# Kernel tuning notes

Hardware: AMD Instinct MI355X
Metric: run time of the kernel (lower is better)

## Reference

```python
import jax, jax.numpy as jnp
import numpy as np
import math

B, S, E, H = 2, 2048, 512, 8
D = E // H
EPS = 1e-6
MAXN = 1.0 - 1e-5  # stay strictly inside the Poincare ball


def _norm(x):
    return jnp.sqrt(jnp.clip(jnp.sum(x * x, axis=-1, keepdims=True), 1e-12))


def expmap0(u):
    n = _norm(u)
    return jnp.tanh(n) * u / n


def logmap0(x):
    n = _norm(x)
    return jnp.arctanh(jnp.clip(n, None, MAXN)) * x / n


def hlinear(x, W, b):
    # HLinear: Mobius matvec == expmap0(W @ logmap0(x)), tangent bias
    return expmap0(logmap0(x) @ W.T + b)


def _lbeta(a, b):
    return math.lgamma(a) + math.lgamma(b) - math.lgamma(a + b)


def setup_inputs() -> dict:
    key = jax.random.key(0)
    ks = jax.random.split(key, 6)

    def pt(k, shape):  # random points on the Poincare ball
        return expmap0(0.2 * jax.random.normal(k, shape, dtype=jnp.float32))

    return {
        "query": pt(ks[0], (B, S, E)),
        "key": pt(ks[1], (B, S, E)),
        "value": pt(ks[2], (B, S, E)),
        "Wq": jax.random.normal(ks[3], (E, E), jnp.float32) / math.sqrt(E),
        "Wk": jax.random.normal(ks[4], (E, E), jnp.float32) / math.sqrt(E),
        "Wv": jax.random.normal(ks[5], (E, E), jnp.float32) / math.sqrt(E),
        "bq": jnp.zeros((E,), jnp.float32),
        "bk": jnp.zeros((E,), jnp.float32),
        "bv": jnp.zeros((E,), jnp.float32),
        "scale_tau": jnp.zeros((1,), jnp.float32),
        "scale_gamma": jnp.zeros((1,), jnp.float32),
    }


def reference(query, key, value, Wq, Wk, Wv, bq, bk, bv, scale_tau, scale_gamma):
    # hyperbolic q/k/v projections, then split heads: [B,H,S,D]
    q = hlinear(query, Wq, bq).reshape(B, S, H, D).transpose(0, 2, 1, 3)
    k = hlinear(key, Wk, bk).reshape(B, S, H, D).transpose(0, 2, 1, 3)
    v = hlinear(value, Wv, bv).reshape(B, S, H, D).transpose(0, 2, 1, 3)

    # pairwise Poincare distance via norms + dot (no [S,S,D] intermediate)
    qn2 = jnp.sum(q * q, -1)                       # [B,H,S]
    kn2 = jnp.sum(k * k, -1)                       # [B,H,S]
    dot = jnp.einsum('bhid,bhjd->bhij', q, k)      # [B,H,S,S]
    sq = jnp.clip(qn2[..., :, None] + kn2[..., None, :] - 2.0 * dot, 0.0)
    denom = jnp.clip((1.0 - qn2)[..., :, None] * (1.0 - kn2)[..., None, :], EPS)
    dist = jnp.arccosh(jnp.clip(1.0 + 2.0 * sq / denom, 1.0 + 1e-7))

    # attention_similarity: -d / tau + gamma, tau = 1/exp(scale_tau)
    sim = -dist * jnp.exp(scale_tau[0]) + scale_gamma[0]

    # causal mask + 'exp' activation (masked_fill(-inf) then exp -> 0)
    mask = jnp.triu(jnp.ones((S, S), bool), 1)
    w = jnp.where(mask, 0.0, jnp.exp(sim))         # [B,H,S,S]

    # gyromidpoint: (1/2) (x) [sum_j w lam_j v_j / sum_j w (lam_j - 1)]
    vn2 = jnp.sum(v * v, -1)
    lam = 2.0 / jnp.clip(1.0 - vn2, EPS)           # [B,H,S]
    num = jnp.einsum('bhij,bhjd->bhid', w, v * lam[..., None])
    den = jnp.einsum('bhij,bhj->bhi', w, lam - 1.0)
    m = num / jnp.clip(den, EPS)[..., None]
    mn = _norm(m)
    mid = jnp.tanh(0.5 * jnp.arctanh(jnp.clip(mn, None, MAXN))) * m / mn

    # beta-concatenation of heads back to embed_dim
    beta_ratio = math.exp(_lbeta(E / 2.0, 0.5) - _lbeta(D / 2.0, 0.5))
    t = logmap0(mid) * beta_ratio                  # [B,H,S,D]
    t = t.transpose(0, 2, 1, 3).reshape(B, S, E)
    return expmap0(t)
```

## Files before the change

### kernel.cpp

```cpp
#include <hip/hip_runtime.h>
#include <cmath>

#define BB 2
#define SS 2048
#define EE 512
#define HH 8
#define DD 64

typedef unsigned short u16t;
typedef __bf16 bf16x8 __attribute__((ext_vector_type(8)));
typedef float f32x4 __attribute__((ext_vector_type(4)));

__device__ __forceinline__ float bf2f(u16t u){
    union{unsigned int i; float f;} c; c.i = ((unsigned int)u)<<16; return c.f;
}
__device__ __forceinline__ u16t f2bf(float x){
    union{float f; unsigned int i;} c; c.f = x;
    return (u16t)((c.i + 0x7fffu + ((c.i>>16)&1u))>>16);
}
__device__ __forceinline__ float fast_tanh(float x){
    float e = __expf(2.f*x); return 1.f - 2.f/(e+1.f);
}
__device__ __forceinline__ float fast_atanh(float x){
    return 0.5f*__logf((1.f+x)/(1.f-x));
}
__device__ __forceinline__ f32x4 mfma16(bf16x8 a, bf16x8 b, f32x4 c){
    return __builtin_amdgcn_mfma_f32_16x16x32_bf16(a,b,c,0,0,0);
}
__device__ __forceinline__ int chunk_off(int qi){
    int g = qi >> 3;
    return (g==1) ? 2*(qi-8) : ((g==2) ? 16 + 3*(qi-16) : 40 + 4*(qi-24));
}

__global__ __launch_bounds__(256) void k_pre(const float* __restrict__ qp,
                                             const float* __restrict__ kp,
                                             const float* __restrict__ vp,
                                             u16t* __restrict__ Tlog,
                                             const float* __restrict__ Wq,
                                             const float* __restrict__ Wk,
                                             const float* __restrict__ Wv,
                                             u16t* __restrict__ Wb){
    int bx = blockIdx.x;
    if (bx < 3072){
        int gr = bx*4 + (threadIdx.x>>6);
        int t = gr >> 12;
        int row = gr & 4095;
        int lane = threadIdx.x & 63;
        const float* src = (t==0 ? qp : (t==1 ? kp : vp)) + (size_t)row*EE;
        const float4* s4 = (const float4*)(src + lane*8);
        float4 a = s4[0], b = s4[1];
        float x[8] = {a.x,a.y,a.z,a.w,b.x,b.y,b.z,b.w};
        float p = 0.f;
        #pragma unroll
        for (int i=0;i<8;++i) p += x[i]*x[i];
        #pragma unroll
        for (int off=32; off>=1; off>>=1) p += __shfl_xor(p, off, 64);
        float n = sqrtf(fmaxf(p, 1e-12f));
        float f = fast_atanh(fminf(n, 1.0f-1e-5f)) / n;
        u16t yb[8];
        #pragma unroll
        for (int i=0;i<8;++i) yb[i] = f2bf(f*x[i]);
        uint4 o;
        o.x = (unsigned)yb[0] | ((unsigned)yb[1]<<16);
        o.y = (unsigned)yb[2] | ((unsigned)yb[3]<<16);
        o.z = (unsigned)yb[4] | ((unsigned)yb[5]<<16);
        o.w = (unsigned)yb[6] | ((unsigned)yb[7]<<16);
        *(uint4*)(Tlog + ((size_t)(t*4096+row)*EE + lane*8)) = o;
    } else {
        int idx = ((bx-3072)*256 + threadIdx.x)*4;
        int t = idx >> 18;
        int off = idx & 262143;
        const float* W = (t==0 ? Wq : (t==1 ? Wk : Wv));
        float4 a = *(const float4*)(W + off);
        uint2 o;
        o.x = (unsigned)f2bf(a.x) | ((unsigned)f2bf(a.y)<<16);
        o.y = (unsigned)f2bf(a.z) | ((unsigned)f2bf(a.w)<<16);
        *(uint2*)(Wb + idx) = o;
    }
}

__global__ __launch_bounds__(256) void k_proj(const u16t* __restrict__ Tlog,
                                              const u16t* __restrict__ Wb,
                                              const float* __restrict__ bq,
                                              const float* __restrict__ bk,
                                              const float* __restrict__ bv,
                                              u16t* __restrict__ U){
    __shared__ __align__(16) u16t Wl[64][72];
    int bx = blockIdx.x;
    int t = bx >> 9; int rem = bx & 511;
    int m0 = (rem >> 3) << 6; int n0 = (rem & 7) << 6;
    int tid = threadIdx.x; int wv = tid>>6; int lane = tid&63;
    int l15 = lane & 15; int l4 = lane >> 4;
    const u16t* Tt = Tlog + (size_t)t*4096*EE;
    const u16t* Wt = Wb + (size_t)t*EE*EE;
    const float* bias = (t==0 ? bq : (t==1 ? bk : bv));
    f32x4 z = {0.f,0.f,0.f,0.f};
    f32x4 acc[4] = {z,z,z,z};
    int arow = m0 + 16*wv + l15;
    for (int ks=0; ks<8; ++ks){
        int k0 = ks*64;
        __syncthreads();
        {
            int rr = tid >> 2; int cc = (tid & 3) * 16;
            const uint4* g = (const uint4*)(Wt + (size_t)(n0+rr)*EE + k0 + cc);
            uint4 w0 = g[0], w1 = g[1];
            *(uint4*)&Wl[rr][cc]   = w0;
            *(uint4*)&Wl[rr][cc+8] = w1;
        }
        __syncthreads();
        bf16x8 a0 = *(const bf16x8*)(Tt + (size_t)arow*EE + k0 + l4*8);
        bf16x8 a1 = *(const bf16x8*)(Tt + (size_t)arow*EE + k0 + 32 + l4*8);
        #pragma unroll
        for (int f=0; f<4; ++f){
            bf16x8 b0 = *(const bf16x8*)&Wl[f*16+l15][l4*8];
            bf16x8 b1 = *(const bf16x8*)&Wl[f*16+l15][32+l4*8];
            acc[f] = mfma16(a0, b0, acc[f]);
            acc[f] = mfma16(a1, b1, acc[f]);
        }
    }
    u16t* Ut = U + (size_t)t*4096*EE;
    #pragma unroll
    for (int f=0; f<4; ++f){
        int col = n0 + f*16 + l15;
        float bs = bias[col];
        #pragma unroll
        for (int r=0; r<4; ++r){
            int row = m0 + 16*wv + l4*4 + r;
            Ut[(size_t)row*EE + col] = f2bf(acc[f][r] + bs);
        }
    }
}

__global__ __launch_bounds__(256) void k_expmap_split(const u16t* __restrict__ U,
        u16t* __restrict__ Q, u16t* __restrict__ K, u16t* __restrict__ VT,
        float* __restrict__ qn2, float* __restrict__ kn2, float* __restrict__ lam1){
    int gr = blockIdx.x*4 + (threadIdx.x>>6);
    int t = gr >> 12;
    int row = gr & 4095;
    int b = row >> 11; int s = row & 2047;
    int lane = threadIdx.x & 63;
    const u16t* u = U + ((size_t)t*4096 + row)*EE;
    uint4 raw = *(const uint4*)(u + lane*8);
    const u16t* rs = (const u16t*)&raw;
    float x[8];
    #pragma unroll
    for (int i=0;i<8;++i) x[i] = bf2f(rs[i]);
    float p = 0.f;
    #pragma unroll
    for (int i=0;i<8;++i) p += x[i]*x[i];
    #pragma unroll
    for (int off=32; off>=1; off>>=1) p += __shfl_xor(p, off, 64);
    float n = sqrtf(fmaxf(p, 1e-12f));
    float f = fast_tanh(n)/n;
    float y[8]; u16t yb[8];
    float hp = 0.f;
    #pragma unroll
    for (int i=0;i<8;++i){
        yb[i] = f2bf(f*x[i]);
        y[i]  = bf2f(yb[i]);
        hp += y[i]*y[i];
    }
    #pragma unroll
    for (int off=1; off<8; off<<=1) hp += __shfl_xor(hp, off, 64);
    hp = fminf(hp, 0.99999988f);
    int h = lane >> 3;
    size_t ih = (size_t)(b*HH + h)*SS + s;
    if (t == 0){
        uint4 o;
        o.x=(unsigned)yb[0]|((unsigned)yb[1]<<16); o.y=(unsigned)yb[2]|((unsigned)yb[3]<<16);
        o.z=(unsigned)yb[4]|((unsigned)yb[5]<<16); o.w=(unsigned)yb[6]|((unsigned)yb[7]<<16);
        *(uint4*)(Q + ih*DD + (lane&7)*8) = o;
        if ((lane&7)==0) qn2[ih] = hp;
    } else if (t == 1){
        uint4 o;
        o.x=(unsigned)yb[0]|((unsigned)yb[1]<<16); o.y=(unsigned)yb[2]|((unsigned)yb[3]<<16);
        o.z=(unsigned)yb[4]|((unsigned)yb[5]<<16); o.w=(unsigned)yb[6]|((unsigned)yb[7]<<16);
        *(uint4*)(K + ih*DD + (lane&7)*8) = o;
        if ((lane&7)==0) kn2[ih] = hp;
    } else {
        float lam = 2.f / fmaxf(1.f - hp, 1e-6f);
        size_t bh = (size_t)(b*HH + h);
        int d0 = (lane&7)*8;
        #pragma unroll
        for (int i=0;i<8;++i)
            VT[(bh*DD + d0 + i)*SS + s] = f2bf(y[i]*lam);
        if ((lane&7)==0) lam1[ih] = lam - 1.f;
    }
}

__global__ __launch_bounds__(256,5) void k_attn(const u16t* __restrict__ Q,
        const u16t* __restrict__ K, const u16t* __restrict__ VT,
        const float* __restrict__ qn2, const float* __restrict__ kn2,
        const float* __restrict__ lam1, const float* __restrict__ taup,
        const float* __restrict__ gammap,
        float* __restrict__ pnum, float* __restrict__ pden,
        float* __restrict__ T2, float beta){
    __shared__ __align__(16) u16t Kt[64][72];
    __shared__ __align__(16) u16t Vt[64][72];
    __shared__ __align__(16) u16t Wt[64][72];
    __shared__ float kn2s[64], lam1s[64], qn2s[64];
    int bx = blockIdx.x;
    int bh = bx & 15;
    int u = bx >> 4;
    int qi, c0;
    if (u < 48){
        int g = u >> 3, r = u & 7;
        int qb = (g==0) ? 8 : ((g<3) ? 16 : 24);
        int cb = (g==0) ? 0 : ((g<3) ? (g-1) : (g-3));
        qi = qb + r; c0 = cb;
    } else {
        int p = u - 48;
        qi = (7 - (p>>2)) + ((p&3)<<3);
        c0 = qi >> 3;
    }
    int jt0 = c0 << 3;
    int jt1 = (u < 48) ? (jt0 + 8) : (qi + 1);
    int s0 = qi << 6;
    int tid = threadIdx.x; int wv = tid>>6; int lane = tid&63;
    int l15 = lane & 15; int l4 = lane >> 4;
    float tauexp = __expf(taup[0]);
    float gm2 = gammap[0] * 1.44269504088896340736f;
    size_t base = (size_t)bh * SS;
    int qrow = s0 + 16*wv + l15;
    bf16x8 aQ0 = *(const bf16x8*)(Q + (base + qrow)*DD + l4*8);
    bf16x8 aQ1 = *(const bf16x8*)(Q + (base + qrow)*DD + 32 + l4*8);
    if (tid < 64) qn2s[tid] = qn2[base + s0 + tid];
    __syncthreads();
    int mloc0 = 16*wv + l4*4;
    float qv_[4], aq2_[4];
    #pragma unroll
    for (int r=0;r<4;++r){
        qv_[r]  = qn2s[mloc0+r];
        aq2_[r] = 2.f * __builtin_amdgcn_rcpf(fmaxf(1.f - qv_[r], 1e-6f));
    }
    f32x4 z4 = {0.f,0.f,0.f,0.f};
    f32x4 num[4] = {z4,z4,z4,z4};
    float den[4] = {0.f,0.f,0.f,0.f};
    int rr = tid >> 2; int cc = (tid & 3) << 4;
    uint4 pka0, pka1, pva0, pva1; float pkn = 0.f, pl1 = 0.f;
    {
        int kv0 = jt0 << 6;
        const uint4* gk = (const uint4*)(K + (base + kv0 + rr)*DD + cc);
        pka0 = gk[0]; pka1 = gk[1];
        const uint4* gv = (const uint4*)(VT + ((size_t)bh*DD + rr)*SS + kv0 + cc);
        pva0 = gv[0]; pva1 = gv[1];
        if (tid < 64){ pkn = kn2[base+kv0+tid]; pl1 = lam1[base+kv0+tid]; }
    }
    for (int jt=jt0; jt<jt1; ++jt){
        *(uint4*)&Kt[rr][cc]   = pka0;
        *(uint4*)&Kt[rr][cc+8] = pka1;
        *(uint4*)&Vt[rr][cc]   = pva0;
        *(uint4*)&Vt[rr][cc+8] = pva1;
        if (tid < 64){ kn2s[tid] = pkn; lam1s[tid] = pl1; }
        __syncthreads();
        if (jt+1 < jt1){
            int kv0n = (jt+1) << 6;
            const uint4* gk = (const uint4*)(K + (base + kv0n + rr)*DD + cc);
            pka0 = gk[0]; pka1 = gk[1];
            const uint4* gv = (const uint4*)(VT + ((size_t)bh*DD + rr)*SS + kv0n + cc);
            pva0 = gv[0]; pva1 = gv[1];
            if (tid < 64){ pkn = kn2[base+kv0n+tid]; pl1 = lam1[base+kv0n+tid]; }
        }
        int kv0 = jt << 6;
        f32x4 c[4] = {z4,z4,z4,z4};
        #pragma unroll
        for (int f=0; f<4; ++f){
            bf16x8 b0 = *(const bf16x8*)&Kt[f*16+l15][l4*8];
            bf16x8 b1 = *(const bf16x8*)&Kt[f*16+l15][32+l4*8];
            c[f] = mfma16(aQ0, b0, c[f]);
            c[f] = mfma16(aQ1, b1, c[f]);
        }
        bool diag = (jt == qi);
        #pragma unroll
        for (int f=0; f<4; ++f){
            int nl = f*16 + l15;
            float kv2 = kn2s[nl];
            float l1  = lam1s[nl];
            float akf = __builtin_amdgcn_rcpf(fmaxf(1.f - kv2, 1e-6f));
            #pragma unroll
            for (int r=0; r<4; ++r){
                int ml = mloc0 + r;
                float sq  = fmaxf(fmaf(-2.f, c[f][r], qv_[r] + kv2), 0.f);
                float co  = fminf(aq2_[r]*akf, 2e6f);
                float rho = fmaxf(sq*co, 1e-7f);
                float tt  = fmaf(rho, rho, rho+rho);
                float zz  = 1.f + rho + __builtin_amdgcn_sqrtf(tt);
                float L   = __builtin_amdgcn_logf(zz);
                float wval= __builtin_amdgcn_exp2f(fmaf(-tauexp, L, gm2));
                if (diag && (kv0+nl) > (s0+ml)) wval = 0.f;
                den[r] = fmaf(wval, l1, den[r]);
                Wt[ml][nl] = f2bf(wval);
            }
        }
        bf16x8 aW0 = *(const bf16x8*)&Wt[16*wv + l15][l4*8];
        bf16x8 aW1 = *(const bf16x8*)&Wt[16*wv + l15][32 + l4*8];
        #pragma unroll
        for (int f=0; f<4; ++f){
            bf16x8 b0 = *(const bf16x8*)&Vt[f*16+l15][l4*8];
            bf16x8 b1 = *(const bf16x8*)&Vt[f*16+l15][32+l4*8];
            num[f] = mfma16(aW0, b0, num[f]);
            num[f] = mfma16(aW1, b1, num[f]);
        }
        __syncthreads();
    }
    #pragma unroll
    for (int r=0; r<4; ++r){
        #pragma unroll
        for (int off=1; off<16; off<<=1) den[r] += __shfl_xor(den[r], off, 64);
    }
    if (qi >= 8){
        size_t pidx = (size_t)bh*72 + chunk_off(qi) + c0;
        float* pn = pnum + pidx*4096;
        #pragma unroll
        for (int f=0; f<4; ++f){
            int nl = f*16 + l15;
            #pragma unroll
            for (int r=0; r<4; ++r)
                pn[(mloc0+r)*64 + nl] = num[f][r];
        }
        if (l15 == 0){
            #pragma unroll
            for (int r=0; r<4; ++r) pden[pidx*64 + mloc0 + r] = den[r];
        }
    } else {
        float mv[4][4]; float mn2[4] = {0.f,0.f,0.f,0.f};
        #pragma unroll
        for (int f=0; f<4; ++f)
            #pragma unroll
            for (int r=0; r<4; ++r){
                mv[f][r] = num[f][r] / fmaxf(den[r], 1e-6f);
                mn2[r] += mv[f][r]*mv[f][r];
            }
        #pragma unroll
        for (int r=0; r<4; ++r){
            #pragma unroll
            for (int off=1; off<16; off<<=1) mn2[r] += __shfl_xor(mn2[r], off, 64);
        }
        int b = bh >> 3; int h = bh & 7;
        #pragma unroll
        for (int r=0; r<4; ++r){
            float mn = sqrtf(fmaxf(mn2[r], 1e-12f));
            float g = beta * 0.5f * fast_atanh(fminf(mn, 1.0f-1e-5f)) / mn;
            int ml = mloc0 + r;
            #pragma unroll
            for (int f=0; f<4; ++f){
                int nl = f*16 + l15;
                T2[((size_t)b*SS + s0 + ml)*EE + h*DD + nl] = g * mv[f][r];
            }
        }
    }
}

__global__ __launch_bounds__(256) void k_combine(const float* __restrict__ pnum,
        const float* __restrict__ pden, float* __restrict__ T2, float beta){
    int bx = blockIdx.x;
    int bh = bx & 15; int qi = 8 + (bx >> 4);
    int nch = (qi >> 3) + 1;
    int t = threadIdx.x; int row = t >> 2; int qd = t & 3;
    size_t pb = (size_t)bh*72 + chunk_off(qi);
    float mv[16];
    #pragma unroll
    for (int i=0;i<16;++i) mv[i] = 0.f;
    float den = 0.f;
    for (int cc=0; cc<nch; ++cc){
        const float* pn = pnum + (pb+cc)*4096 + row*64 + qd*16;
        #pragma unroll
        for (int i=0;i<4;++i){
            float4 v = *(const float4*)(pn + i*4);
            mv[i*4+0]+=v.x; mv[i*4+1]+=v.y; mv[i*4+2]+=v.z; mv[i*4+3]+=v.w;
        }
        den += pden[(pb+cc)*64 + row];
    }
    float invd = 1.f / fmaxf(den, 1e-6f);
    float mn2 = 0.f;
    #pragma unroll
    for (int i=0;i<16;++i){ mv[i] *= invd; mn2 += mv[i]*mv[i]; }
    mn2 += __shfl_xor(mn2, 1, 64);
    mn2 += __shfl_xor(mn2, 2, 64);
    float mn = sqrtf(fmaxf(mn2, 1e-12f));
    float g = beta * 0.5f * fast_atanh(fminf(mn, 1.0f-1e-5f)) / mn;
    int b = bh >> 3, h = bh & 7;
    float* dst = T2 + ((size_t)b*SS + (qi<<6) + row)*EE + h*DD + qd*16;
    #pragma unroll
    for (int i=0;i<4;++i){
        float4 v = {g*mv[i*4+0], g*mv[i*4+1], g*mv[i*4+2], g*mv[i*4+3]};
        *(float4*)(dst + i*4) = v;
    }
}

__global__ __launch_bounds__(256) void k_final(const float* __restrict__ T2,
                                               float* __restrict__ out){
    int row = blockIdx.x*4 + (threadIdx.x>>6);
    int lane = threadIdx.x & 63;
    const float* src = T2 + (size_t)row*EE;
    const float4* s4 = (const float4*)(src + lane*8);
    float4 a = s4[0], b = s4[1];
    float x[8] = {a.x,a.y,a.z,a.w,b.x,b.y,b.z,b.w};
    float p = 0.f;
    #pragma unroll
    for (int i=0;i<8;++i) p += x[i]*x[i];
    #pragma unroll
    for (int off=32; off>=1; off>>=1) p += __shfl_xor(p, off, 64);
    float n = sqrtf(fmaxf(p, 1e-12f));
    float f = fast_tanh(n)/n;
    float4 o0 = {f*x[0], f*x[1], f*x[2], f*x[3]};
    float4 o1 = {f*x[4], f*x[5], f*x[6], f*x[7]};
    float4* d4 = (float4*)(out + (size_t)row*EE + lane*8);
    d4[0] = o0; d4[1] = o1;
}

extern "C" void kernel_launch(void* const* d_in, const int* in_sizes, int n_in,
                              void* d_out, int out_size, void* d_ws, size_t ws_size,
                              hipStream_t stream) {
    const float* q_in  = (const float*)d_in[0];
    const float* k_in  = (const float*)d_in[1];
    const float* v_in  = (const float*)d_in[2];
    const float* Wq    = (const float*)d_in[3];
    const float* Wk    = (const float*)d_in[4];
    const float* Wv    = (const float*)d_in[5];
    const float* bq    = (const float*)d_in[6];
    const float* bk    = (const float*)d_in[7];
    const float* bv    = (const float*)d_in[8];
    const float* tau   = (const float*)d_in[9];
    const float* gamma = (const float*)d_in[10];
    float* out = (float*)d_out;

    char* ws = (char*)d_ws;
    u16t*  Tlog = (u16t*)(ws + 0);
    u16t*  Wb   = (u16t*)(ws + 12582912);
    u16t*  Ub   = (u16t*)(ws + 14155776);
    u16t*  Qb   = (u16t*)(ws + 26738688);
    u16t*  Kb   = (u16t*)(ws + 30932992);
    u16t*  VTb  = (u16t*)(ws + 35127296);
    float* qn2  = (float*)(ws + 39321600);
    float* kn2  = (float*)(ws + 39452672);
    float* lam1 = (float*)(ws + 39583744);
    float* pnum = (float*)(ws + 0);
    float* pden = (float*)(ws + 18874368);
    float* T2   = (float*)(ws + 39714816);

    double lb1 = std::lgamma(256.0) + std::lgamma(0.5) - std::lgamma(256.5);
    double lb2 = std::lgamma(32.0)  + std::lgamma(0.5) - std::lgamma(32.5);
    float beta = (float)std::exp(lb1 - lb2);

    k_pre<<<3840, 256, 0, stream>>>(q_in, k_in, v_in, Tlog, Wq, Wk, Wv, Wb);
    k_proj<<<1536, 256, 0, stream>>>(Tlog, Wb, bq, bk, bv, Ub);
    k_expmap_split<<<3072, 256, 0, stream>>>(Ub, Qb, Kb, VTb, qn2, kn2, lam1);
    k_attn<<<1280, 256, 0, stream>>>(Qb, Kb, VTb, qn2, kn2, lam1, tau, gamma,
                                     pnum, pden, T2, beta);
    k_combine<<<384, 256, 0, stream>>>(pnum, pden, T2, beta);
    k_final<<<1024, 256, 0, stream>>>(T2, out);
}
```

Measured before the change: 97.49 us.

## Split attention into 4-tile KV chunks, read K/V directly, prefetch W in projection

```diff
diff --git a/kernel.cpp b/kernel.cpp
--- a/kernel.cpp
+++ b/kernel.cpp
@@ -27,9 +27,9 @@
 __device__ __forceinline__ f32x4 mfma16(bf16x8 a, bf16x8 b, f32x4 c){
     return __builtin_amdgcn_mfma_f32_16x16x32_bf16(a,b,c,0,0,0);
 }
-__device__ __forceinline__ int chunk_off(int qi){
-    int g = qi >> 3;
-    return (g==1) ? 2*(qi-8) : ((g==2) ? 16 + 3*(qi-16) : 40 + 4*(qi-24));
+__device__ __forceinline__ int coff4(int qi){
+    int a = qi >> 2, b = qi & 3;
+    return 2*a*(a+1) - 4 + b*(a+1);
 }
 
 __global__ __launch_bounds__(256) void k_pre(const float* __restrict__ qp,
@@ -97,17 +97,21 @@
     f32x4 z = {0.f,0.f,0.f,0.f};
     f32x4 acc[4] = {z,z,z,z};
     int arow = m0 + 16*wv + l15;
+    int rr = tid >> 2; int cc = (tid & 3) * 16;
+    uint4 w0, w1;
+    {
+        const uint4* g = (const uint4*)(Wt + (size_t)(n0+rr)*EE + cc);
+        w0 = g[0]; w1 = g[1];
+    }
     for (int ks=0; ks<8; ++ks){
         int k0 = ks*64;
+        *(uint4*)&Wl[rr][cc]   = w0;
+        *(uint4*)&Wl[rr][cc+8] = w1;
         __syncthreads();
-        {
-            int rr = tid >> 2; int cc = (tid & 3) * 16;
-            const uint4* g = (const uint4*)(Wt + (size_t)(n0+rr)*EE + k0 + cc);
-            uint4 w0 = g[0], w1 = g[1];
-            *(uint4*)&Wl[rr][cc]   = w0;
-            *(uint4*)&Wl[rr][cc+8] = w1;
-        }
-        __syncthreads();
+        if (ks < 7){
+            const uint4* g = (const uint4*)(Wt + (size_t)(n0+rr)*EE + k0 + 64 + cc);
+            w0 = g[0]; w1 = g[1];
+        }
         bf16x8 a0 = *(const bf16x8*)(Tt + (size_t)arow*EE + k0 + l4*8);
         bf16x8 a1 = *(const bf16x8*)(Tt + (size_t)arow*EE + k0 + 32 + l4*8);
         #pragma unroll
@@ -117,6 +121,7 @@
             acc[f] = mfma16(a0, b0, acc[f]);
             acc[f] = mfma16(a1, b1, acc[f]);
         }
+        __syncthreads();
     }
     u16t* Ut = U + (size_t)t*4096*EE;
     #pragma unroll
@@ -188,33 +193,31 @@
     }
 }
 
-__global__ __launch_bounds__(256,5) void k_attn(const u16t* __restrict__ Q,
+__global__ __launch_bounds__(256,6) void k_attn(const u16t* __restrict__ Q,
         const u16t* __restrict__ K, const u16t* __restrict__ VT,
         const float* __restrict__ qn2, const float* __restrict__ kn2,
         const float* __restrict__ lam1, const float* __restrict__ taup,
         const float* __restrict__ gammap,
         float* __restrict__ pnum, float* __restrict__ pden,
         float* __restrict__ T2, float beta){
-    __shared__ __align__(16) u16t Kt[64][72];
-    __shared__ __align__(16) u16t Vt[64][72];
     __shared__ __align__(16) u16t Wt[64][72];
-    __shared__ float kn2s[64], lam1s[64], qn2s[64];
     int bx = blockIdx.x;
     int bh = bx & 15;
     int u = bx >> 4;
     int qi, c0;
-    if (u < 48){
-        int g = u >> 3, r = u & 7;
-        int qb = (g==0) ? 8 : ((g<3) ? 16 : 24);
-        int cb = (g==0) ? 0 : ((g<3) ? (g-1) : (g-3));
-        qi = qb + r; c0 = cb;
+    if (u < 140){
+        int v = 139 - u;
+        int a = 1;
+        while (2*(a+1)*(a+2)-4 <= v) ++a;
+        int rem = v - (2*a*(a+1)-4);
+        int b_ = rem / (a+1);
+        c0 = rem - b_*(a+1);
+        qi = 4*a + b_;
     } else {
-        int p = u - 48;
-        qi = (7 - (p>>2)) + ((p&3)<<3);
-        c0 = qi >> 3;
-    }
-    int jt0 = c0 << 3;
-    int jt1 = (u < 48) ? (jt0 + 8) : (qi + 1);
+        qi = u - 140; c0 = 0;
+    }
+    int jt0 = c0 << 2;
+    int jt1 = min(jt0 + 4, qi + 1);
     int s0 = qi << 6;
     int tid = threadIdx.x; int wv = tid>>6; int lane = tid&63;
     int l15 = lane & 15; int l4 = lane >> 4;
@@ -224,58 +227,43 @@
     int qrow = s0 + 16*wv + l15;
     bf16x8 aQ0 = *(const bf16x8*)(Q + (base + qrow)*DD + l4*8);
     bf16x8 aQ1 = *(const bf16x8*)(Q + (base + qrow)*DD + 32 + l4*8);
-    if (tid < 64) qn2s[tid] = qn2[base + s0 + tid];
-    __syncthreads();
     int mloc0 = 16*wv + l4*4;
     float qv_[4], aq2_[4];
     #pragma unroll
     for (int r=0;r<4;++r){
-        qv_[r]  = qn2s[mloc0+r];
+        qv_[r]  = qn2[base + s0 + mloc0 + r];
         aq2_[r] = 2.f * __builtin_amdgcn_rcpf(fmaxf(1.f - qv_[r], 1e-6f));
     }
     f32x4 z4 = {0.f,0.f,0.f,0.f};
     f32x4 num[4] = {z4,z4,z4,z4};
     float den[4] = {0.f,0.f,0.f,0.f};
-    int rr = tid >> 2; int cc = (tid & 3) << 4;
-    uint4 pka0, pka1, pva0, pva1; float pkn = 0.f, pl1 = 0.f;
-    {
-        int kv0 = jt0 << 6;
-        const uint4* gk = (const uint4*)(K + (base + kv0 + rr)*DD + cc);
-        pka0 = gk[0]; pka1 = gk[1];
-        const uint4* gv = (const uint4*)(VT + ((size_t)bh*DD + rr)*SS + kv0 + cc);
-        pva0 = gv[0]; pva1 = gv[1];
-        if (tid < 64){ pkn = kn2[base+kv0+tid]; pl1 = lam1[base+kv0+tid]; }
-    }
     for (int jt=jt0; jt<jt1; ++jt){
-        *(uint4*)&Kt[rr][cc]   = pka0;
-        *(uint4*)&Kt[rr][cc+8] = pka1;
-        *(uint4*)&Vt[rr][cc]   = pva0;
-        *(uint4*)&Vt[rr][cc+8] = pva1;
-        if (tid < 64){ kn2s[tid] = pkn; lam1s[tid] = pl1; }
-        __syncthreads();
-        if (jt+1 < jt1){
-            int kv0n = (jt+1) << 6;
-            const uint4* gk = (const uint4*)(K + (base + kv0n + rr)*DD + cc);
-            pka0 = gk[0]; pka1 = gk[1];
-            const uint4* gv = (const uint4*)(VT + ((size_t)bh*DD + rr)*SS + kv0n + cc);
-            pva0 = gv[0]; pva1 = gv[1];
-            if (tid < 64){ pkn = kn2[base+kv0n+tid]; pl1 = lam1[base+kv0n+tid]; }
-        }
         int kv0 = jt << 6;
+        const u16t* Kp = K + (base + kv0)*DD;
+        const u16t* Vp = VT + ((size_t)bh*DD)*SS + kv0;
+        float kn2v[4], l1v[4];
         f32x4 c[4] = {z4,z4,z4,z4};
         #pragma unroll
         for (int f=0; f<4; ++f){
-            bf16x8 b0 = *(const bf16x8*)&Kt[f*16+l15][l4*8];
-            bf16x8 b1 = *(const bf16x8*)&Kt[f*16+l15][32+l4*8];
-            c[f] = mfma16(aQ0, b0, c[f]);
-            c[f] = mfma16(aQ1, b1, c[f]);
+            kn2v[f] = kn2[base + kv0 + f*16 + l15];
+            l1v[f]  = lam1[base + kv0 + f*16 + l15];
+            bf16x8 kb0 = *(const bf16x8*)(Kp + (f*16+l15)*DD + l4*8);
+            bf16x8 kb1 = *(const bf16x8*)(Kp + (f*16+l15)*DD + 32 + l4*8);
+            c[f] = mfma16(aQ0, kb0, c[f]);
+            c[f] = mfma16(aQ1, kb1, c[f]);
+        }
+        bf16x8 vb0[4], vb1[4];
+        #pragma unroll
+        for (int f=0; f<4; ++f){
+            vb0[f] = *(const bf16x8*)(Vp + (size_t)(f*16+l15)*SS + l4*8);
+            vb1[f] = *(const bf16x8*)(Vp + (size_t)(f*16+l15)*SS + 32 + l4*8);
         }
         bool diag = (jt == qi);
         #pragma unroll
         for (int f=0; f<4; ++f){
             int nl = f*16 + l15;
-            float kv2 = kn2s[nl];
-            float l1  = lam1s[nl];
+            float kv2 = kn2v[f];
+            float l1  = l1v[f];
             float akf = __builtin_amdgcn_rcpf(fmaxf(1.f - kv2, 1e-6f));
             #pragma unroll
             for (int r=0; r<4; ++r){
@@ -296,20 +284,17 @@
         bf16x8 aW1 = *(const bf16x8*)&Wt[16*wv + l15][32 + l4*8];
         #pragma unroll
         for (int f=0; f<4; ++f){
-            bf16x8 b0 = *(const bf16x8*)&Vt[f*16+l15][l4*8];
-            bf16x8 b1 = *(const bf16x8*)&Vt[f*16+l15][32+l4*8];
-            num[f] = mfma16(aW0, b0, num[f]);
-            num[f] = mfma16(aW1, b1, num[f]);
-        }
-        __syncthreads();
+            num[f] = mfma16(aW0, vb0[f], num[f]);
+            num[f] = mfma16(aW1, vb1[f], num[f]);
+        }
     }
     #pragma unroll
     for (int r=0; r<4; ++r){
         #pragma unroll
         for (int off=1; off<16; off<<=1) den[r] += __shfl_xor(den[r], off, 64);
     }
-    if (qi >= 8){
-        size_t pidx = (size_t)bh*72 + chunk_off(qi) + c0;
+    if (qi >= 4){
+        size_t pidx = (size_t)bh*140 + coff4(qi) + c0;
         float* pn = pnum + pidx*4096;
         #pragma unroll
         for (int f=0; f<4; ++f){
@@ -354,10 +339,10 @@
 __global__ __launch_bounds__(256) void k_combine(const float* __restrict__ pnum,
         const float* __restrict__ pden, float* __restrict__ T2, float beta){
     int bx = blockIdx.x;
-    int bh = bx & 15; int qi = 8 + (bx >> 4);
-    int nch = (qi >> 3) + 1;
+    int bh = bx & 15; int qi = 4 + (bx >> 4);
+    int nch = (qi >> 2) + 1;
     int t = threadIdx.x; int row = t >> 2; int qd = t & 3;
-    size_t pb = (size_t)bh*72 + chunk_off(qi);
+    size_t pb = (size_t)bh*140 + coff4(qi);
     float mv[16];
     #pragma unroll
     for (int i=0;i<16;++i) mv[i] = 0.f;
@@ -435,9 +420,9 @@
     float* qn2  = (float*)(ws + 39321600);
     float* kn2  = (float*)(ws + 39452672);
     float* lam1 = (float*)(ws + 39583744);
-    float* pnum = (float*)(ws + 0);
-    float* pden = (float*)(ws + 18874368);
-    float* T2   = (float*)(ws + 39714816);
+    float* pnum = (float*)(ws + 39714816);
+    float* pden = (float*)(ws + 76414976);
+    float* T2   = (float*)(ws + 76988416);
 
     double lb1 = std::lgamma(256.0) + std::lgamma(0.5) - std::lgamma(256.5);
     double lb2 = std::lgamma(32.0)  + std::lgamma(0.5) - std::lgamma(32.5);
@@ -446,8 +431,8 @@
     k_pre<<<3840, 256, 0, stream>>>(q_in, k_in, v_in, Tlog, Wq, Wk, Wv, Wb);
     k_proj<<<1536, 256, 0, stream>>>(Tlog, Wb, bq, bk, bv, Ub);
     k_expmap_split<<<3072, 256, 0, stream>>>(Ub, Qb, Kb, VTb, qn2, kn2, lam1);
-    k_attn<<<1280, 256, 0, stream>>>(Qb, Kb, VTb, qn2, kn2, lam1, tau, gamma,
+    k_attn<<<2304, 256, 0, stream>>>(Qb, Kb, VTb, qn2, kn2, lam1, tau, gamma,
                                      pnum, pden, T2, beta);
-    k_combine<<<384, 256, 0, stream>>>(pnum, pden, T2, beta);
+    k_combine<<<448, 256, 0, stream>>>(pnum, pden, T2, beta);
     k_final<<<1024, 256, 0, stream>>>(T2, out);
 }
```

New measurement: 156.6 us. 1.61x slower.

## Use 128-row query tiles in attention and fuse combine with final expmap

Applied to the files above, without the earlier changes.

```diff
diff --git a/kernel.cpp b/kernel.cpp
--- a/kernel.cpp
+++ b/kernel.cpp
@@ -27,9 +27,10 @@
 __device__ __forceinline__ f32x4 mfma16(bf16x8 a, bf16x8 b, f32x4 c){
     return __builtin_amdgcn_mfma_f32_16x16x32_bf16(a,b,c,0,0,0);
 }
-__device__ __forceinline__ int chunk_off(int qi){
-    int g = qi >> 3;
-    return (g==1) ? 2*(qi-8) : ((g==2) ? 16 + 3*(qi-16) : 40 + 4*(qi-24));
+__device__ __forceinline__ int nch128(int qb){ return (qb+2)>>1; }
+__device__ __forceinline__ int off128(int qb){
+    int m = qb>>1;
+    return (qb & 1) ? (m+1)*(m+1) : m*(m+1);
 }
 
 __global__ __launch_bounds__(256) void k_pre(const float* __restrict__ qp,
@@ -97,17 +98,21 @@
     f32x4 z = {0.f,0.f,0.f,0.f};
     f32x4 acc[4] = {z,z,z,z};
     int arow = m0 + 16*wv + l15;
+    int rr = tid >> 2; int cc = (tid & 3) * 16;
+    uint4 w0, w1;
+    {
+        const uint4* g = (const uint4*)(Wt + (size_t)(n0+rr)*EE + cc);
+        w0 = g[0]; w1 = g[1];
+    }
     for (int ks=0; ks<8; ++ks){
         int k0 = ks*64;
+        *(uint4*)&Wl[rr][cc]   = w0;
+        *(uint4*)&Wl[rr][cc+8] = w1;
         __syncthreads();
-        {
-            int rr = tid >> 2; int cc = (tid & 3) * 16;
-            const uint4* g = (const uint4*)(Wt + (size_t)(n0+rr)*EE + k0 + cc);
-            uint4 w0 = g[0], w1 = g[1];
-            *(uint4*)&Wl[rr][cc]   = w0;
-            *(uint4*)&Wl[rr][cc+8] = w1;
-        }
-        __syncthreads();
+        if (ks < 7){
+            const uint4* g = (const uint4*)(Wt + (size_t)(n0+rr)*EE + k0 + 64 + cc);
+            w0 = g[0]; w1 = g[1];
+        }
         bf16x8 a0 = *(const bf16x8*)(Tt + (size_t)arow*EE + k0 + l4*8);
         bf16x8 a1 = *(const bf16x8*)(Tt + (size_t)arow*EE + k0 + 32 + l4*8);
         #pragma unroll
@@ -117,6 +122,7 @@
             acc[f] = mfma16(a0, b0, acc[f]);
             acc[f] = mfma16(a1, b1, acc[f]);
         }
+        __syncthreads();
     }
     u16t* Ut = U + (size_t)t*4096*EE;
     #pragma unroll
@@ -188,54 +194,48 @@
     }
 }
 
-__global__ __launch_bounds__(256,5) void k_attn(const u16t* __restrict__ Q,
+__global__ __launch_bounds__(256,3) void k_attn(const u16t* __restrict__ Q,
         const u16t* __restrict__ K, const u16t* __restrict__ VT,
         const float* __restrict__ qn2, const float* __restrict__ kn2,
         const float* __restrict__ lam1, const float* __restrict__ taup,
         const float* __restrict__ gammap,
-        float* __restrict__ pnum, float* __restrict__ pden,
-        float* __restrict__ T2, float beta){
+        float* __restrict__ pnum, float* __restrict__ pden){
     __shared__ __align__(16) u16t Kt[64][72];
     __shared__ __align__(16) u16t Vt[64][72];
     __shared__ __align__(16) u16t Wt[64][72];
-    __shared__ float kn2s[64], lam1s[64], qn2s[64];
+    __shared__ float kn2s[64], lam1s[64];
     int bx = blockIdx.x;
     int bh = bx & 15;
     int u = bx >> 4;
-    int qi, c0;
-    if (u < 48){
-        int g = u >> 3, r = u & 7;
-        int qb = (g==0) ? 8 : ((g<3) ? 16 : 24);
-        int cb = (g==0) ? 0 : ((g<3) ? (g-1) : (g-3));
-        qi = qb + r; c0 = cb;
-    } else {
-        int p = u - 48;
-        qi = (7 - (p>>2)) + ((p&3)<<3);
-        c0 = qi >> 3;
-    }
-    int jt0 = c0 << 3;
-    int jt1 = (u < 48) ? (jt0 + 8) : (qi + 1);
-    int s0 = qi << 6;
+    int v = 71 - u;
+    int qb = 15;
+    while (off128(qb) > v) --qb;
+    int c0 = v - off128(qb);
+    int jt0 = c0 << 2;
+    int jt1 = min(jt0 + 4, 2*qb + 2);
+    int s0 = qb << 7;
     int tid = threadIdx.x; int wv = tid>>6; int lane = tid&63;
     int l15 = lane & 15; int l4 = lane >> 4;
     float tauexp = __expf(taup[0]);
     float gm2 = gammap[0] * 1.44269504088896340736f;
     size_t base = (size_t)bh * SS;
-    int qrow = s0 + 16*wv + l15;
-    bf16x8 aQ0 = *(const bf16x8*)(Q + (base + qrow)*DD + l4*8);
-    bf16x8 aQ1 = *(const bf16x8*)(Q + (base + qrow)*DD + 32 + l4*8);
-    if (tid < 64) qn2s[tid] = qn2[base + s0 + tid];
-    __syncthreads();
     int mloc0 = 16*wv + l4*4;
-    float qv_[4], aq2_[4];
-    #pragma unroll
-    for (int r=0;r<4;++r){
-        qv_[r]  = qn2s[mloc0+r];
-        aq2_[r] = 2.f * __builtin_amdgcn_rcpf(fmaxf(1.f - qv_[r], 1e-6f));
+    bf16x8 aQ0[2], aQ1[2];
+    float qv_[2][4], aq2_[2][4];
+    #pragma unroll
+    for (int rb=0; rb<2; ++rb){
+        int qrow = s0 + rb*64 + 16*wv + l15;
+        aQ0[rb] = *(const bf16x8*)(Q + (base + qrow)*DD + l4*8);
+        aQ1[rb] = *(const bf16x8*)(Q + (base + qrow)*DD + 32 + l4*8);
+        #pragma unroll
+        for (int r=0;r<4;++r){
+            qv_[rb][r]  = qn2[base + s0 + rb*64 + mloc0 + r];
+            aq2_[rb][r] = 2.f * __builtin_amdgcn_rcpf(fmaxf(1.f - qv_[rb][r], 1e-6f));
+        }
     }
     f32x4 z4 = {0.f,0.f,0.f,0.f};
-    f32x4 num[4] = {z4,z4,z4,z4};
-    float den[4] = {0.f,0.f,0.f,0.f};
+    f32x4 num[2][4] = {{z4,z4,z4,z4},{z4,z4,z4,z4}};
+    float den[2][4] = {{0.f,0.f,0.f,0.f},{0.f,0.f,0.f,0.f}};
     int rr = tid >> 2; int cc = (tid & 3) << 4;
     uint4 pka0, pka1, pva0, pva1; float pkn = 0.f, pl1 = 0.f;
     {
@@ -262,151 +262,119 @@
             if (tid < 64){ pkn = kn2[base+kv0n+tid]; pl1 = lam1[base+kv0n+tid]; }
         }
         int kv0 = jt << 6;
-        f32x4 c[4] = {z4,z4,z4,z4};
-        #pragma unroll
-        for (int f=0; f<4; ++f){
-            bf16x8 b0 = *(const bf16x8*)&Kt[f*16+l15][l4*8];
-            bf16x8 b1 = *(const bf16x8*)&Kt[f*16+l15][32+l4*8];
-            c[f] = mfma16(aQ0, b0, c[f]);
-            c[f] = mfma16(aQ1, b1, c[f]);
-        }
-        bool diag = (jt == qi);
+        #pragma unroll
+        for (int rb=0; rb<2; ++rb){
+            if (jt > 2*qb + rb) continue;
+            f32x4 c[4] = {z4,z4,z4,z4};
+            #pragma unroll
+            for (int f=0; f<4; ++f){
+                bf16x8 b0 = *(const bf16x8*)&Kt[f*16+l15][l4*8];
+                bf16x8 b1 = *(const bf16x8*)&Kt[f*16+l15][32+l4*8];
+                c[f] = mfma16(aQ0[rb], b0, c[f]);
+                c[f] = mfma16(aQ1[rb], b1, c[f]);
+            }
+            bool diag = (jt == 2*qb + rb);
+            int qrow0 = s0 + rb*64 + mloc0;
+            #pragma unroll
+            for (int f=0; f<4; ++f){
+                int nl = f*16 + l15;
+                float kv2 = kn2s[nl];
+                float l1  = lam1s[nl];
+                float akf = __builtin_amdgcn_rcpf(fmaxf(1.f - kv2, 1e-6f));
+                #pragma unroll
+                for (int r=0; r<4; ++r){
+                    float sq  = fmaxf(fmaf(-2.f, c[f][r], qv_[rb][r] + kv2), 0.f);
+                    float co  = fminf(aq2_[rb][r]*akf, 2e6f);
+                    float rho = fmaxf(sq*co, 1e-7f);
+                    float tt  = fmaf(rho, rho, rho+rho);
+                    float zz  = 1.f + rho + __builtin_amdgcn_sqrtf(tt);
+                    float L   = __builtin_amdgcn_logf(zz);
+                    float wval= __builtin_amdgcn_exp2f(fmaf(-tauexp, L, gm2));
+                    if (diag && (kv0+nl) > (qrow0+r)) wval = 0.f;
+                    den[rb][r] = fmaf(wval, l1, den[rb][r]);
+                    Wt[mloc0 + r][nl] = f2bf(wval);
+                }
+            }
+            bf16x8 aW0 = *(const bf16x8*)&Wt[16*wv + l15][l4*8];
+            bf16x8 aW1 = *(const bf16x8*)&Wt[16*wv + l15][32 + l4*8];
+            #pragma unroll
+            for (int f=0; f<4; ++f){
+                bf16x8 b0 = *(const bf16x8*)&Vt[f*16+l15][l4*8];
+                bf16x8 b1 = *(const bf16x8*)&Vt[f*16+l15][32+l4*8];
+                num[rb][f] = mfma16(aW0, b0, num[rb][f]);
+                num[rb][f] = mfma16(aW1, b1, num[rb][f]);
+            }
+        }
+        __syncthreads();
+    }
+    size_t pidx = (size_t)bh*72 + off128(qb) + c0;
+    float* pn = pnum + pidx*8192;
+    #pragma unroll
+    for (int rb=0; rb<2; ++rb){
+        #pragma unroll
+        for (int r=0; r<4; ++r){
+            #pragma unroll
+            for (int off=1; off<16; off<<=1)
+                den[rb][r] += __shfl_xor(den[rb][r], off, 64);
+        }
         #pragma unroll
         for (int f=0; f<4; ++f){
             int nl = f*16 + l15;
-            float kv2 = kn2s[nl];
-            float l1  = lam1s[nl];
-            float akf = __builtin_amdgcn_rcpf(fmaxf(1.f - kv2, 1e-6f));
-            #pragma unroll
-            for (int r=0; r<4; ++r){
-                int ml = mloc0 + r;
-                float sq  = fmaxf(fmaf(-2.f, c[f][r], qv_[r] + kv2), 0.f);
-                float co  = fminf(aq2_[r]*akf, 2e6f);
-                float rho = fmaxf(sq*co, 1e-7f);
-                float tt  = fmaf(rho, rho, rho+rho);
-                float zz  = 1.f + rho + __builtin_amdgcn_sqrtf(tt);
-                float L   = __builtin_amdgcn_logf(zz);
-                float wval= __builtin_amdgcn_exp2f(fmaf(-tauexp, L, gm2));
-                if (diag && (kv0+nl) > (s0+ml)) wval = 0.f;
-                den[r] = fmaf(wval, l1, den[r]);
-                Wt[ml][nl] = f2bf(wval);
-            }
-        }
-        bf16x8 aW0 = *(const bf16x8*)&Wt[16*wv + l15][l4*8];
-        bf16x8 aW1 = *(const bf16x8*)&Wt[16*wv + l15][32 + l4*8];
-        #pragma unroll
-        for (int f=0; f<4; ++f){
-            bf16x8 b0 = *(const bf16x8*)&Vt[f*16+l15][l4*8];
-            bf16x8 b1 = *(const bf16x8*)&Vt[f*16+l15][32+l4*8];
-            num[f] = mfma16(aW0, b0, num[f]);
-            num[f] = mfma16(aW1, b1, num[f]);
-        }
-        __syncthreads();
-    }
-    #pragma unroll
-    for (int r=0; r<4; ++r){
-        #pragma unroll
-        for (int off=1; off<16; off<<=1) den[r] += __shfl_xor(den[r], off, 64);
-    }
-    if (qi >= 8){
-        size_t pidx = (size_t)bh*72 + chunk_off(qi) + c0;
-        float* pn = pnum + pidx*4096;
-        #pragma unroll
-        for (int f=0; f<4; ++f){
-            int nl = f*16 + l15;
             #pragma unroll
             for (int r=0; r<4; ++r)
-                pn[(mloc0+r)*64 + nl] = num[f][r];
+                pn[(rb*64 + mloc0 + r)*64 + nl] = num[rb][f][r];
         }
         if (l15 == 0){
             #pragma unroll
-            for (int r=0; r<4; ++r) pden[pidx*64 + mloc0 + r] = den[r];
-        }
-    } else {
-        float mv[4][4]; float mn2[4] = {0.f,0.f,0.f,0.f};
-        #pragma unroll
-        for (int f=0; f<4; ++f)
-            #pragma unroll
-            for (int r=0; r<4; ++r){
-                mv[f][r] = num[f][r] / fmaxf(den[r], 1e-6f);
-                mn2[r] += mv[f][r]*mv[f][r];
-            }
-        #pragma unroll
-        for (int r=0; r<4; ++r){
-            #pragma unroll
-            for (int off=1; off<16; off<<=1) mn2[r] += __shfl_xor(mn2[r], off, 64);
-        }
-        int b = bh >> 3; int h = bh & 7;
-        #pragma unroll
-        for (int r=0; r<4; ++r){
-            float mn = sqrtf(fmaxf(mn2[r], 1e-12f));
-            float g = beta * 0.5f * fast_atanh(fminf(mn, 1.0f-1e-5f)) / mn;
-            int ml = mloc0 + r;
-            #pragma unroll
-            for (int f=0; f<4; ++f){
-                int nl = f*16 + l15;
-                T2[((size_t)b*SS + s0 + ml)*EE + h*DD + nl] = g * mv[f][r];
-            }
-        }
-    }
-}
-
-__global__ __launch_bounds__(256) void k_combine(const float* __restrict__ pnum,
-        const float* __restrict__ pden, float* __restrict__ T2, float beta){
+            for (int r=0; r<4; ++r)
+                pden[pidx*128 + rb*64 + mloc0 + r] = den[rb][r];
+        }
+    }
+}
+
+__global__ __launch_bounds__(256) void k_post(const float* __restrict__ pnum,
+        const float* __restrict__ pden, float* __restrict__ out, float beta){
     int bx = blockIdx.x;
-    int bh = bx & 15; int qi = 8 + (bx >> 4);
-    int nch = (qi >> 3) + 1;
-    int t = threadIdx.x; int row = t >> 2; int qd = t & 3;
-    size_t pb = (size_t)bh*72 + chunk_off(qi);
-    float mv[16];
-    #pragma unroll
-    for (int i=0;i<16;++i) mv[i] = 0.f;
+    int b = bx >> 7; int stile = bx & 127;
+    int tid = threadIdx.x;
+    int row = tid >> 4; int h = (tid >> 1) & 7; int half = tid & 1;
+    int s = stile*16 + row;
+    int qb = s >> 7; int rowin = s & 127;
+    int nch = nch128(qb);
+    size_t pb = (size_t)(b*HH + h)*72 + off128(qb);
+    float mv[32];
+    #pragma unroll
+    for (int i=0;i<32;++i) mv[i] = 0.f;
     float den = 0.f;
     for (int cc=0; cc<nch; ++cc){
-        const float* pn = pnum + (pb+cc)*4096 + row*64 + qd*16;
-        #pragma unroll
-        for (int i=0;i<4;++i){
+        const float* pn = pnum + (pb+cc)*8192 + rowin*64 + half*32;
+        #pragma unroll
+        for (int i=0;i<8;++i){
             float4 v = *(const float4*)(pn + i*4);
             mv[i*4+0]+=v.x; mv[i*4+1]+=v.y; mv[i*4+2]+=v.z; mv[i*4+3]+=v.w;
         }
-        den += pden[(pb+cc)*64 + row];
+        den += pden[(pb+cc)*128 + rowin];
     }
     float invd = 1.f / fmaxf(den, 1e-6f);
-    float mn2 = 0.f;
-    #pragma unroll
-    for (int i=0;i<16;++i){ mv[i] *= invd; mn2 += mv[i]*mv[i]; }
-    mn2 += __shfl_xor(mn2, 1, 64);
-    mn2 += __shfl_xor(mn2, 2, 64);
+    float mn2h = 0.f;
+    #pragma unroll
+    for (int i=0;i<32;++i){ mv[i] *= invd; mn2h += mv[i]*mv[i]; }
+    float mn2 = mn2h + __shfl_xor(mn2h, 1, 64);
     float mn = sqrtf(fmaxf(mn2, 1e-12f));
     float g = beta * 0.5f * fast_atanh(fminf(mn, 1.0f-1e-5f)) / mn;
-    int b = bh >> 3, h = bh & 7;
-    float* dst = T2 + ((size_t)b*SS + (qi<<6) + row)*EE + h*DD + qd*16;
-    #pragma unroll
-    for (int i=0;i<4;++i){
-        float4 v = {g*mv[i*4+0], g*mv[i*4+1], g*mv[i*4+2], g*mv[i*4+3]};
+    float tn = g*g*mn2;
+    tn += __shfl_xor(tn, 2, 64);
+    tn += __shfl_xor(tn, 4, 64);
+    tn += __shfl_xor(tn, 8, 64);
+    float en = sqrtf(fmaxf(tn, 1e-12f));
+    float f = fast_tanh(en)/en;
+    float gf = g * f;
+    float* dst = out + ((size_t)(b*SS + s))*EE + h*DD + half*32;
+    #pragma unroll
+    for (int i=0;i<8;++i){
+        float4 v = {gf*mv[i*4+0], gf*mv[i*4+1], gf*mv[i*4+2], gf*mv[i*4+3]};
         *(float4*)(dst + i*4) = v;
     }
-}
-
-__global__ __launch_bounds__(256) void k_final(const float* __restrict__ T2,
-                                               float* __restrict__ out){
-    int row = blockIdx.x*4 + (threadIdx.x>>6);
-    int lane = threadIdx.x & 63;
-    const float* src = T2 + (size_t)row*EE;
-    const float4* s4 = (const float4*)(src + lane*8);
-    float4 a = s4[0], b = s4[1];
-    float x[8] = {a.x,a.y,a.z,a.w,b.x,b.y,b.z,b.w};
-    float p = 0.f;
-    #pragma unroll
-    for (int i=0;i<8;++i) p += x[i]*x[i];
-    #pragma unroll
-    for (int off=32; off>=1; off>>=1) p += __shfl_xor(p, off, 64);
-    float n = sqrtf(fmaxf(p, 1e-12f));
-    float f = fast_tanh(n)/n;
-    float4 o0 = {f*x[0], f*x[1], f*x[2], f*x[3]};
-    float4 o1 = {f*x[4], f*x[5], f*x[6], f*x[7]};
-    float4* d4 = (float4*)(out + (size_t)row*EE + lane*8);
-    d4[0] = o0; d4[1] = o1;
 }
 
 extern "C" void kernel_launch(void* const* d_in, const int* in_sizes, int n_in,
@@ -435,9 +403,8 @@
     float* qn2  = (float*)(ws + 39321600);
     float* kn2  = (float*)(ws + 39452672);
     float* lam1 = (float*)(ws + 39583744);
-    float* pnum = (float*)(ws + 0);
-    float* pden = (float*)(ws + 18874368);
-    float* T2   = (float*)(ws + 39714816);
+    float* pnum = (float*)(ws + 39714816);
+    float* pden = (float*)(ws + 77463552);
 
     double lb1 = std::lgamma(256.0) + std::lgamma(0.5) - std::lgamma(256.5);
     double lb2 = std::lgamma(32.0)  + std::lgamma(0.5) - std::lgamma(32.5);
@@ -446,8 +413,7 @@
     k_pre<<<3840, 256, 0, stream>>>(q_in, k_in, v_in, Tlog, Wq, Wk, Wv, Wb);
     k_proj<<<1536, 256, 0, stream>>>(Tlog, Wb, bq, bk, bv, Ub);
     k_expmap_split<<<3072, 256, 0, stream>>>(Ub, Qb, Kb, VTb, qn2, kn2, lam1);
-    k_attn<<<1280, 256, 0, stream>>>(Qb, Kb, VTb, qn2, kn2, lam1, tau, gamma,
-                                     pnum, pden, T2, beta);
-    k_combine<<<384, 256, 0, stream>>>(pnum, pden, T2, beta);
-    k_final<<<1024, 256, 0, stream>>>(T2, out);
-}
+    k_attn<<<1152, 256, 0, stream>>>(Qb, Kb, VTb, qn2, kn2, lam1, tau, gamma,
+                                     pnum, pden);
+    k_post<<<256, 256, 0, stream>>>(pnum, pden, out, beta);
+}
```

Result: slower. 103.9 us (+6.6%).
